# Kernel optimization log

Measured on AMD Instinct MI355X. Metric: run time of the kernel, lower is better.

The kernel has to match this reference:

```python
import jax, jax.numpy as jnp
import numpy as np

# dims: E=2 experts, R=64 lora rank, IN=768, HID=3072, OUT=768, B=32, S=1280 (chunks 256+1024)
SCALE = 128.0 / 64.0  # lora_alpha / lora_rank


def setup_inputs() -> dict:
    key = jax.random.key(0)
    ks = jax.random.split(key, 9)
    B, S, IN, HID, OUT, E, R = 32, 1280, 768, 3072, 768, 2, 64
    inp = {
        "x": jax.random.normal(ks[0], (B, S, IN), jnp.float32),
        "w1": jax.random.normal(ks[1], (HID, IN), jnp.float32) * 0.02,
        "bias1": jax.random.normal(ks[2], (HID,), jnp.float32) * 0.02,
        "a1": jax.random.normal(ks[3], (E, R, IN), jnp.float32) * 0.02,
        "b1": jax.random.normal(ks[4], (E, HID, R), jnp.float32) * 0.02,
        "w2": jax.random.normal(ks[5], (OUT, HID), jnp.float32) * 0.02,
        "bias2": jax.random.normal(ks[6], (OUT,), jnp.float32) * 0.02,
        "a2": jax.random.normal(ks[7], (E, R, HID), jnp.float32) * 0.02,
        "b2": jax.random.normal(ks[8], (E, OUT, R), jnp.float32) * 0.02,
        "expert_indices": np.array([0, 1], dtype=np.int64),
        "chunk_sizes": np.array([256, 1024], dtype=np.int64),
    }
    return inp


def _lora_linear(x, w, bias, a_e, b_e):
    # y = x @ W^T + b + scale * (x @ A^T) @ B^T   (LoRA, dropout=0)
    return x @ w.T + bias + SCALE * ((x @ a_e.T) @ b_e.T)


def reference(x, w1, bias1, a1, b1, w2, bias2, a2, b2, expert_indices, chunk_sizes):
    sizes = [int(s) for s in np.asarray(chunk_sizes)]
    eids = [int(e) for e in np.asarray(expert_indices)]
    outs = []
    start = 0
    for sz, e in zip(sizes, eids):
        xc = x[:, start:start + sz]  # [B, sz, IN] static slice
        start += sz
        h = _lora_linear(xc, w1, bias1, a1[e], b1[e])
        h = jax.nn.gelu(h, approximate=False)  # nn.GELU default (erf)
        y = _lora_linear(h, w2, bias2, a2[e], b2[e])
        outs.append(y)
    return jnp.concatenate(outs, axis=1)
```

## Files before the change

kernel.cpp:

```cpp
#include <hip/hip_runtime.h>

typedef __attribute__((ext_vector_type(8))) short short8;
typedef __attribute__((ext_vector_type(4))) float f32x4;

__device__ __forceinline__ unsigned short f2bf(float f) {
  union { float f; unsigned u; } v; v.f = f;
  unsigned r = v.u + 0x7fffu + ((v.u >> 16) & 1u);
  return (unsigned short)(r >> 16);
}

__device__ __forceinline__ void async16(const void* g, void* l) {
  __builtin_amdgcn_global_load_lds(
      (const __attribute__((address_space(1))) unsigned*)g,
      (__attribute__((address_space(3))) unsigned*)l, 16, 0, 0);
}

#define MEMFENCE() asm volatile("" ::: "memory")
#define BARRIER() __builtin_amdgcn_s_barrier()
#define WAIT_VM(N) asm volatile("s_waitcnt vmcnt(" #N ")" ::: "memory")

__device__ __forceinline__ float gelu_exact(float v) {
  float s = v * 0.70710678118f;
  float x = fabsf(s);
  float t = 1.0f / (1.0f + 0.3275911f * x);
  float p = t * (0.254829592f +
            t * (-0.284496736f +
            t * (1.421413741f + t * (-1.453152027f + t * 1.061405429f))));
  float er = 1.0f - p * __expf(-x * x);
  er = copysignf(er, s);
  return 0.5f * v * (1.0f + er);
}

__global__ void cvt_bf16_kernel(const float4* __restrict__ in,
                                ushort4* __restrict__ out, int n4) {
  int i = blockIdx.x * blockDim.x + threadIdx.x;
  int stride = gridDim.x * blockDim.x;
  for (; i < n4; i += stride) {
    float4 v = in[i];
    ushort4 o;
    o.x = f2bf(v.x); o.y = f2bf(v.y); o.z = f2bf(v.z); o.w = f2bf(v.w);
    out[i] = o;
  }
}

__global__ void make_weff(const float* __restrict__ w,
                          const float* __restrict__ bmat,
                          const float* __restrict__ amat,
                          unsigned short* __restrict__ out,
                          int J, int K) {
  const int e = blockIdx.y;
  const float* a = amat + (size_t)e * 64 * K;
  const float* b = bmat + (size_t)e * J * 64;
  const int j0 = blockIdx.x * 16;
  __shared__ float bs[16][64];
  const int tid = threadIdx.x;
  for (int i = tid; i < 16 * 64; i += 256)
    bs[i >> 6][i & 63] = b[(size_t)(j0 + (i >> 6)) * 64 + (i & 63)];
  __syncthreads();
  for (int k = tid; k < K; k += 256) {
    float acc[16];
#pragma unroll
    for (int jj = 0; jj < 16; ++jj) acc[jj] = 0.f;
    for (int r = 0; r < 64; ++r) {
      float av = a[(size_t)r * K + k];
#pragma unroll
      for (int jj = 0; jj < 16; ++jj) acc[jj] += bs[jj][r] * av;
    }
#pragma unroll
    for (int jj = 0; jj < 16; ++jj) {
      float v = w[(size_t)(j0 + jj) * K + k] + 2.0f * acc[jj];
      out[((size_t)e * J + j0 + jj) * K + k] = f2bf(v);
    }
  }
}


#define STAGE_A(Xs, ob)                                                        \
  do {                                                                         \
    const char* _g = (const char*)Ap + gbyte + (ob);                           \
    async16(_g, (Xs) + loff);                                                  \
    async16(_g + (size_t)K * 256, (Xs) + loff + 4096);                         \
  } while (0)
#define STAGE_B(Xs, ob) async16((const char*)Bp + gbyte + (ob), (Xs) + loff)

template <bool FUSE_GELU, bool OUT_BF16>
__global__ __launch_bounds__(512, 4) void gemm128(
    const unsigned short* __restrict__ A, const unsigned short* __restrict__ Bw,
    const float* __restrict__ bias, void* __restrict__ Cout, int N, int K,
    int NXT) {
  extern __shared__ unsigned short lds[];
  unsigned short* Abuf0 = lds;
  unsigned short* Abuf1 = lds + 8192;
  unsigned short* Abuf2 = lds + 16384;
  unsigned short* Bbuf0 = lds + 24576;
  unsigned short* Bbuf1 = lds + 28672;
  unsigned short* Bbuf2 = lds + 32768;

  const int tid = threadIdx.x;
  const int w = tid >> 6, lane = tid & 63;

  const int nwg = gridDim.x, bid = blockIdx.x;
  const int qchunk = nwg >> 3;
  const int wg = (bid & 7) * qchunk + (bid >> 3);
  const int by = wg / NXT, bx = wg - by * NXT;
  const int m0 = by << 8, n0 = bx << 7;
  const int e = (m0 % 1280) ? 1 : 0;
  const unsigned short* Ap = A + (size_t)m0 * K;
  const unsigned short* Bp = Bw + ((size_t)e * N + n0) * K;

  const int wr = w >> 1, wc = w & 1;
  const int fr = lane & 15;
  const int cbv = (((lane >> 4) ^ ((fr >> 1) & 3)) << 4);
  const int arowB = (wr * 64 + fr) * 64;
  const int browB = (wc * 64 + fr) * 64;

  const int sslot = (lane & 3) ^ ((lane >> 3) & 3);
  const size_t gbyte = (size_t)(w * 16 + (lane >> 2)) * K * 2 + sslot * 16;
  const int loff = w * 512;

  f32x4 acc[4][4] = {};
  short8 afm[4], bfv[4];

  const int T = K >> 5;
  const int KB2 = K << 1;

  unsigned short *Ac = Abuf0, *An = Abuf1, *Af = Abuf2;
  unsigned short *Bc = Bbuf0, *Bn = Bbuf1, *Bf = Bbuf2;

  STAGE_A(Abuf0, 0); STAGE_B(Bbuf0, 0);
  STAGE_A(Abuf1, 64); STAGE_B(Bbuf1, 64);
  WAIT_VM(3); MEMFENCE(); BARRIER(); MEMFENCE();

  int ob = 128;

  for (int t = 0; t < T; ++t) {
    STAGE_A(Af, ob); STAGE_B(Bf, ob);
#pragma unroll
    for (int m_ = 0; m_ < 4; ++m_)
      afm[m_] = *(const short8*)((const char*)Ac + arowB + m_ * 1024 + cbv);
#pragma unroll
    for (int n_ = 0; n_ < 4; ++n_)
      bfv[n_] = *(const short8*)((const char*)Bc + browB + n_ * 1024 + cbv);
    __builtin_amdgcn_s_setprio(1);
#pragma unroll
    for (int m_ = 0; m_ < 4; ++m_)
#pragma unroll
      for (int n_ = 0; n_ < 4; ++n_)
        acc[m_][n_] = __builtin_amdgcn_mfma_f32_16x16x32_bf16(
            afm[m_], bfv[n_], acc[m_][n_], 0, 0, 0);
    __builtin_amdgcn_s_setprio(0);
    WAIT_VM(3); MEMFENCE(); BARRIER(); MEMFENCE();
    unsigned short* tA = Ac; Ac = An; An = Af; Af = tA;
    unsigned short* tB = Bc; Bc = Bn; Bn = Bf; Bf = tB;
    ob += 64; if (ob >= KB2) ob -= KB2;
  }

  const int lrow = (lane >> 4) << 2;
#pragma unroll
  for (int mi = 0; mi < 4; ++mi) {
    const int rbase = m0 + wr * 64 + mi * 16 + lrow;
#pragma unroll
    for (int n = 0; n < 4; ++n) {
      const int col = n0 + wc * 64 + n * 16 + fr;
      const float bv = bias[col];
#pragma unroll
      for (int j = 0; j < 4; ++j) {
        const int row = rbase + j;
        float v = acc[mi][n][j] + bv;
        if (FUSE_GELU) v = gelu_exact(v);
        if (OUT_BF16)
          ((unsigned short*)Cout)[(size_t)row * N + col] = f2bf(v);
        else
          ((float*)Cout)[(size_t)row * N + col] = v;
      }
    }
  }
}

extern "C" void kernel_launch(void* const* d_in, const int* in_sizes, int n_in,
                              void* d_out, int out_size, void* d_ws,
                              size_t ws_size, hipStream_t stream) {
  const float* x = (const float*)d_in[0];
  const float* w1 = (const float*)d_in[1];
  const float* bias1 = (const float*)d_in[2];
  const float* a1 = (const float*)d_in[3];
  const float* b1 = (const float*)d_in[4];
  const float* w2 = (const float*)d_in[5];
  const float* bias2 = (const float*)d_in[6];
  const float* a2 = (const float*)d_in[7];
  const float* b2 = (const float*)d_in[8];
  float* out = (float*)d_out;

  char* ws = (char*)d_ws;
  unsigned short* x_bf = (unsigned short*)(ws + 0);
  unsigned short* w1e = (unsigned short*)(ws + 62914560);
  unsigned short* w2e = (unsigned short*)(ws + 72351744);
  unsigned short* h = (unsigned short*)(ws + 81788928);

  hipFuncSetAttribute(reinterpret_cast<const void*>(&gemm128<true, true>),
                      hipFuncAttributeMaxDynamicSharedMemorySize, 73728);
  hipFuncSetAttribute(reinterpret_cast<const void*>(&gemm128<false, false>),
                      hipFuncAttributeMaxDynamicSharedMemorySize, 73728);

  cvt_bf16_kernel<<<4096, 256, 0, stream>>>((const float4*)x, (ushort4*)x_bf,
                                            40960 * 768 / 4);
  make_weff<<<dim3(3072 / 16, 2), 256, 0, stream>>>(w1, b1, a1, w1e, 3072, 768);
  make_weff<<<dim3(768 / 16, 2), 256, 0, stream>>>(w2, b2, a2, w2e, 768, 3072);

  gemm128<true, true><<<3840, 512, 73728, stream>>>(x_bf, w1e, bias1, h, 3072,
                                                    768, 24);
  gemm128<false, false><<<960, 512, 73728, stream>>>(h, w2e, bias2, out, 768,
                                                     3072, 6);
}
```

Before: 754.7 us.

## Use 4 waves per block with 128x64 warp tiles and 3x unrolled triple-buffer loop

The GEMM block drops from 8 waves to 4, so each wave computes a 128x64 sub-tile (8x4 MFMA fragments) of the same 256x128 block tile. Register reuse per LDS fragment load goes up and per-wave overhead goes down. The K loop is unrolled by three with compile-time buffer slot indices, which removes the pointer rotation and offset wraparound, and each thread now issues more async global-to-LDS loads per stage. The cost is twice the accumulator registers, lower occupancy (launch bounds 256,2), and fewer waves available to hide latency.

```diff
diff --git a/kernel.cpp b/kernel.cpp
--- a/kernel.cpp
+++ b/kernel.cpp
@@ -75,26 +75,38 @@
 }
 
 
-#define STAGE_A(Xs, ob)                                                        \
+#define SLOT(J, a0, a1, a2, a3, b0, b1)                                        \
   do {                                                                         \
-    const char* _g = (const char*)Ap + gbyte + (ob);                           \
-    async16(_g, (Xs) + loff);                                                  \
-    async16(_g + (size_t)K * 256, (Xs) + loff + 4096);                         \
+    constexpr int SD = ((J) + 2) % 3;                                          \
+    constexpr int GO = (J) * 64 + 128;                                         \
+    async16(a0 + GO, ldsA + SD * 8192 + ldst);                                 \
+    async16(a1 + GO, ldsA + SD * 8192 + 2048 + ldst);                          \
+    async16(a2 + GO, ldsA + SD * 8192 + 4096 + ldst);                          \
+    async16(a3 + GO, ldsA + SD * 8192 + 6144 + ldst);                          \
+    async16(b0 + GO, ldsB + SD * 4096 + ldst);                                 \
+    async16(b1 + GO, ldsB + SD * 4096 + 2048 + ldst);                          \
+    short8 afm[8], bfv[4];                                                     \
+    _Pragma("unroll") for (int n_ = 0; n_ < 4; ++n_)                           \
+        bfv[n_] = *(const short8*)(bRd + (J) * 8192 + n_ * 1024);              \
+    _Pragma("unroll") for (int m_ = 0; m_ < 8; ++m_)                           \
+        afm[m_] = *(const short8*)(aRd + (J) * 16384 + m_ * 1024);             \
+    __builtin_amdgcn_s_setprio(1);                                             \
+    _Pragma("unroll") for (int m_ = 0; m_ < 8; ++m_)                           \
+    _Pragma("unroll") for (int n_ = 0; n_ < 4; ++n_)                           \
+        acc[m_][n_] = __builtin_amdgcn_mfma_f32_16x16x32_bf16(                 \
+            afm[m_], bfv[n_], acc[m_][n_], 0, 0, 0);                           \
+    __builtin_amdgcn_s_setprio(0);                                             \
+    WAIT_VM(6); MEMFENCE(); BARRIER(); MEMFENCE();                             \
   } while (0)
-#define STAGE_B(Xs, ob) async16((const char*)Bp + gbyte + (ob), (Xs) + loff)
 
 template <bool FUSE_GELU, bool OUT_BF16>
-__global__ __launch_bounds__(512, 4) void gemm128(
+__global__ __launch_bounds__(256, 2) void gemm128(
     const unsigned short* __restrict__ A, const unsigned short* __restrict__ Bw,
     const float* __restrict__ bias, void* __restrict__ Cout, int N, int K,
     int NXT) {
   extern __shared__ unsigned short lds[];
-  unsigned short* Abuf0 = lds;
-  unsigned short* Abuf1 = lds + 8192;
-  unsigned short* Abuf2 = lds + 16384;
-  unsigned short* Bbuf0 = lds + 24576;
-  unsigned short* Bbuf1 = lds + 28672;
-  unsigned short* Bbuf2 = lds + 32768;
+  unsigned short* ldsA = lds;
+  unsigned short* ldsB = lds + 24576;
 
   const int tid = threadIdx.x;
   const int w = tid >> 6, lane = tid & 63;
@@ -111,54 +123,59 @@
   const int wr = w >> 1, wc = w & 1;
   const int fr = lane & 15;
   const int cbv = (((lane >> 4) ^ ((fr >> 1) & 3)) << 4);
-  const int arowB = (wr * 64 + fr) * 64;
-  const int browB = (wc * 64 + fr) * 64;
-
-  const int sslot = (lane & 3) ^ ((lane >> 3) & 3);
-  const size_t gbyte = (size_t)(w * 16 + (lane >> 2)) * K * 2 + sslot * 16;
-  const int loff = w * 512;
-
-  f32x4 acc[4][4] = {};
-  short8 afm[4], bfv[4];
+  const char* aRd = (const char*)lds + (wr * 128 + fr) * 64 + cbv;
+  const char* bRd = (const char*)lds + 49152 + (wc * 64 + fr) * 64 + cbv;
+
+  const int sslot = (tid & 3) ^ ((tid >> 3) & 3);
+  const size_t grow = (size_t)(tid >> 2) * K * 2 + sslot * 16;
+  const size_t KP = (size_t)K * 128;
+  const char* gA0 = (const char*)Ap + grow;
+  const char* gA1 = gA0 + KP;
+  const char* gA2 = gA0 + 2 * KP;
+  const char* gA3 = gA0 + 3 * KP;
+  const char* gB0 = (const char*)Bp + grow;
+  const char* gB1 = gB0 + KP;
+  const int ldst = w * 512;
+
+  f32x4 acc[8][4] = {};
 
   const int T = K >> 5;
+  const int G = T / 3;
   const int KB2 = K << 1;
 
-  unsigned short *Ac = Abuf0, *An = Abuf1, *Af = Abuf2;
-  unsigned short *Bc = Bbuf0, *Bn = Bbuf1, *Bf = Bbuf2;
-
-  STAGE_A(Abuf0, 0); STAGE_B(Bbuf0, 0);
-  STAGE_A(Abuf1, 64); STAGE_B(Bbuf1, 64);
-  WAIT_VM(3); MEMFENCE(); BARRIER(); MEMFENCE();
-
-  int ob = 128;
-
-  for (int t = 0; t < T; ++t) {
-    STAGE_A(Af, ob); STAGE_B(Bf, ob);
-#pragma unroll
-    for (int m_ = 0; m_ < 4; ++m_)
-      afm[m_] = *(const short8*)((const char*)Ac + arowB + m_ * 1024 + cbv);
-#pragma unroll
-    for (int n_ = 0; n_ < 4; ++n_)
-      bfv[n_] = *(const short8*)((const char*)Bc + browB + n_ * 1024 + cbv);
-    __builtin_amdgcn_s_setprio(1);
-#pragma unroll
-    for (int m_ = 0; m_ < 4; ++m_)
-#pragma unroll
-      for (int n_ = 0; n_ < 4; ++n_)
-        acc[m_][n_] = __builtin_amdgcn_mfma_f32_16x16x32_bf16(
-            afm[m_], bfv[n_], acc[m_][n_], 0, 0, 0);
-    __builtin_amdgcn_s_setprio(0);
-    WAIT_VM(3); MEMFENCE(); BARRIER(); MEMFENCE();
-    unsigned short* tA = Ac; Ac = An; An = Af; Af = tA;
-    unsigned short* tB = Bc; Bc = Bn; Bn = Bf; Bf = tB;
-    ob += 64; if (ob >= KB2) ob -= KB2;
+  async16(gA0, ldsA + ldst);
+  async16(gA1, ldsA + 2048 + ldst);
+  async16(gA2, ldsA + 4096 + ldst);
+  async16(gA3, ldsA + 6144 + ldst);
+  async16(gB0, ldsB + ldst);
+  async16(gB1, ldsB + 2048 + ldst);
+  async16(gA0 + 64, ldsA + 8192 + ldst);
+  async16(gA1 + 64, ldsA + 10240 + ldst);
+  async16(gA2 + 64, ldsA + 12288 + ldst);
+  async16(gA3 + 64, ldsA + 14336 + ldst);
+  async16(gB0 + 64, ldsB + 4096 + ldst);
+  async16(gB1 + 64, ldsB + 6144 + ldst);
+  WAIT_VM(6); MEMFENCE(); BARRIER(); MEMFENCE();
+
+  for (int g = 0; g < G - 1; ++g) {
+    SLOT(0, gA0, gA1, gA2, gA3, gB0, gB1);
+    SLOT(1, gA0, gA1, gA2, gA3, gB0, gB1);
+    SLOT(2, gA0, gA1, gA2, gA3, gB0, gB1);
+    gA0 += 192; gA1 += 192; gA2 += 192; gA3 += 192; gB0 += 192; gB1 += 192;
+  }
+  {
+    SLOT(0, gA0, gA1, gA2, gA3, gB0, gB1);
+    const char* wA0 = gA0 - KB2; const char* wA1 = gA1 - KB2;
+    const char* wA2 = gA2 - KB2; const char* wA3 = gA3 - KB2;
+    const char* wB0 = gB0 - KB2; const char* wB1 = gB1 - KB2;
+    SLOT(1, wA0, wA1, wA2, wA3, wB0, wB1);
+    SLOT(2, wA0, wA1, wA2, wA3, wB0, wB1);
   }
 
   const int lrow = (lane >> 4) << 2;
 #pragma unroll
-  for (int mi = 0; mi < 4; ++mi) {
-    const int rbase = m0 + wr * 64 + mi * 16 + lrow;
+  for (int mi = 0; mi < 8; ++mi) {
+    const int rbase = m0 + wr * 128 + mi * 16 + lrow;
 #pragma unroll
     for (int n = 0; n < 4; ++n) {
       const int col = n0 + wc * 64 + n * 16 + fr;
@@ -207,8 +224,8 @@
   make_weff<<<dim3(3072 / 16, 2), 256, 0, stream>>>(w1, b1, a1, w1e, 3072, 768);
   make_weff<<<dim3(768 / 16, 2), 256, 0, stream>>>(w2, b2, a2, w2e, 768, 3072);
 
-  gemm128<true, true><<<3840, 512, 73728, stream>>>(x_bf, w1e, bias1, h, 3072,
+  gemm128<true, true><<<3840, 256, 73728, stream>>>(x_bf, w1e, bias1, h, 3072,
                                                     768, 24);
-  gemm128<false, false><<<960, 512, 73728, stream>>>(h, w2e, bias2, out, 768,
+  gemm128<false, false><<<960, 256, 73728, stream>>>(h, w2e, bias2, out, 768,
                                                      3072, 6);
 }
```

Measured after the change: 744.1 us. Within noise of the previous version (-1.4%).
